# Optimization experiments

Measured on AMD Instinct MI355X. Metric: run time of the kernel, lower is better.

Reference implementation:

```python
import jax, jax.numpy as jnp
import numpy as np

N_HEAD = 8
HID = 256
V_DIM = HID // N_HEAD
IN_CH = 3
OUT_CH = 1
N_BLOCKS = 4
BATCH = 4
N_FULL = 4096
N_LAT = 1024
LOCALITIES = (3.0, 5.0, 5.0, 5.0, 5.0, 3.0)


def _linear(x, w, b):
    # eqx.nn.Linear convention: w is [out, in]
    return x @ w.T + b


def _pos_att(m_dist, x, r, weight, locality):
    # m_dist: [h, Nq, Nk]; x: [b, Nk, HID]; r: [h,1,1]; weight: [h, HID, V_DIM]
    scale = jnp.tan(0.25 * jnp.pi * (1 - 1e-07) * (1 + jnp.sin(r)))  # [h,1,1]
    sd = m_dist * scale  # [h, Nq, Nk]
    if locality <= 100:
        thr = jnp.percentile(sd, locality, axis=-1, keepdims=True)
        sd = jnp.where(sd <= thr, sd, jnp.inf)
    att = jax.nn.softmax(-sd, axis=-1)  # [h, Nq, Nk]
    value = jnp.einsum('bnj,hjk->bhnk', x, weight)  # [b, h, Nk, V_DIM]
    out = jnp.einsum('hjn,bhnk->bhjk', att, value)  # [b, h, Nq, V_DIM]
    out = out.transpose(0, 2, 1, 3).reshape(out.shape[0], out.shape[2], -1)  # [b, Nq, HID]
    return jax.nn.gelu(out)


def setup_inputs():
    key = jax.random.key(0)
    ks = jax.random.split(key, 16)
    def nrm(k, shape, scale=1.0):
        return jax.random.normal(k, shape, dtype=jnp.float32) * scale
    inv = float(1.0 / np.sqrt(HID))
    return {
        'x': nrm(ks[0], (BATCH, N_FULL, IN_CH)),
        'm_dist_down': jax.random.uniform(ks[1], (N_HEAD, N_LAT, N_FULL), dtype=jnp.float32),
        'm_dist_blocks': jax.random.uniform(ks[2], (N_BLOCKS, N_HEAD, N_LAT, N_LAT), dtype=jnp.float32),
        'm_dist_up': jax.random.uniform(ks[3], (N_HEAD, N_FULL, N_LAT), dtype=jnp.float32),
        'en_w': nrm(ks[4], (HID, IN_CH), float(1.0 / np.sqrt(IN_CH))),
        'en_b': jnp.zeros((HID,), jnp.float32),
        'down_r': nrm(ks[5], (N_HEAD, 1, 1)),
        'down_w': nrm(ks[6], (N_HEAD, HID, V_DIM), inv),
        'pa_r': nrm(ks[7], (N_BLOCKS, N_HEAD, 1, 1)),
        'pa_w': nrm(ks[8], (N_BLOCKS, N_HEAD, HID, V_DIM), inv),
        'mlp1_w': nrm(ks[9], (N_BLOCKS, HID, HID), inv),
        'mlp1_b': jnp.zeros((N_BLOCKS, HID), jnp.float32),
        'mlp2_w': nrm(ks[10], (N_BLOCKS, HID, HID), inv),
        'mlp2_b': jnp.zeros((N_BLOCKS, HID), jnp.float32),
        'res_w': nrm(ks[11], (N_BLOCKS, HID, HID), inv),
        'res_b': jnp.zeros((N_BLOCKS, HID), jnp.float32),
        'up_r': nrm(ks[12], (N_HEAD, 1, 1)),
        'up_w': nrm(ks[13], (N_HEAD, HID, V_DIM), inv),
        'de1_w': nrm(ks[14], (HID, HID), inv),
        'de1_b': jnp.zeros((HID,), jnp.float32),
        'de2_w': nrm(ks[15], (OUT_CH, HID), inv),
        'de2_b': jnp.zeros((OUT_CH,), jnp.float32),
    }


def reference(x, m_dist_down, m_dist_blocks, m_dist_up, en_w, en_b, down_r, down_w,
              pa_r, pa_w, mlp1_w, mlp1_b, mlp2_w, mlp2_b, res_w, res_b,
              up_r, up_w, de1_w, de1_b, de2_w, de2_b):
    # Encoder: lift + downsampling position-attention
    h = jax.nn.gelu(_linear(x, en_w, en_b))  # [b, N_FULL, HID]
    h = _pos_att(m_dist_down, h, down_r, down_w, LOCALITIES[0])  # [b, N_LAT, HID]
    # Processor blocks: PA -> MLP, plus linear residual, gelu
    for i in range(N_BLOCKS):
        pa = _pos_att(m_dist_blocks[i], h, pa_r[i], pa_w[i], LOCALITIES[1 + i])
        mlp = _linear(jax.nn.gelu(_linear(pa, mlp1_w[i], mlp1_b[i])), mlp2_w[i], mlp2_b[i])
        h = jax.nn.gelu(mlp + _linear(h, res_w[i], res_b[i]))
    # Decoder: upsampling position-attention + projection
    h = _pos_att(m_dist_up, h, up_r, up_w, LOCALITIES[-1])  # [b, N_FULL, HID]
    h = jax.nn.gelu(_linear(h, de1_w, de1_b))
    return _linear(h, de2_w, de2_b)  # [b, N_FULL, OUT_CH]
```

## Files before the change

kernel.cpp:

```cpp
#include <hip/hip_runtime.h>
#include <math.h>


typedef short bf16x8 __attribute__((ext_vector_type(8)));
typedef float f32x4 __attribute__((ext_vector_type(4)));

__device__ __forceinline__ float gelu_f(float x) {
  float x3 = x * x * x;
  float inner = x + 0.044715f * x3;
  float t = tanhf(0.7978845608028654f * inner);
  return x * (0.5f * (1.0f + t));
}

__device__ __forceinline__ unsigned short f2bf(float x) {
  union { float f; unsigned u; } v; v.f = x;
  return (unsigned short)((v.u + 0x7fffu + ((v.u >> 16) & 1u)) >> 16);
}
__device__ __forceinline__ float bf2f(unsigned short b) {
  union { unsigned u; float f; } v; v.u = ((unsigned)b) << 16; return v.f;
}
__device__ __forceinline__ void store_bf(unsigned short* hi, unsigned short* lo,
                                         size_t i, float v) {
  unsigned short h = f2bf(v);
  hi[i] = h;
  lo[i] = f2bf(v - bf2f(h));
}

struct PrepArgs {
  const float *mlp1, *mlp2, *res, *de1, *down, *pa, *up;
  unsigned short *rm_hi, *rm_lo, *val_hi, *val_lo;
};
__global__ __launch_bounds__(256) void k_prep(PrepArgs p) {
  int i = blockIdx.x * 256 + threadIdx.x;
  if (i < 851968) {
    const float* src; int off;
    if (i < 262144)      { src = p.mlp1; off = i; }
    else if (i < 524288) { src = p.mlp2; off = i - 262144; }
    else if (i < 786432) { src = p.res;  off = i - 524288; }
    else                 { src = p.de1;  off = i - 786432; }
    float x = src[off];
    store_bf(p.rm_hi, p.rm_lo, i, x);
  } else if (i < 1245184) {
    int ii = i - 851968;
    const float* src; int off;
    if (ii < 65536)       { src = p.down; off = ii; }
    else if (ii < 327680) { src = p.pa;   off = ii - 65536; }
    else                  { src = p.up;   off = ii - 327680; }
    int m = off >> 16, rem = off & 65535;
    int o = rem >> 8, j = rem & 255;
    float x = src[(size_t)m * 65536 + (o >> 5) * 8192 + j * 32 + (o & 31)];
    store_bf(p.val_hi, p.val_lo, ii, x);
  }
}

__global__ __launch_bounds__(256) void k_lift(const float* __restrict__ x,
                                              const float* __restrict__ w,
                                              const float* __restrict__ b,
                                              unsigned short* __restrict__ ohi,
                                              unsigned short* __restrict__ olo) {
  int gid = blockIdx.x * 256 + threadIdx.x;
  int m = gid >> 8, o = gid & 255;
  float a0 = x[m * 3 + 0], a1 = x[m * 3 + 1], a2 = x[m * 3 + 2];
  float acc = a0 * w[o * 3 + 0] + a1 * w[o * 3 + 1] + a2 * w[o * 3 + 2] + b[o];
  store_bf(ohi, olo, gid, gelu_f(acc));
}

template <int ACT, int ADDRES, int OBF16>
__global__ __launch_bounds__(256) void k_gemm(
    const unsigned short* __restrict__ Ahi, const unsigned short* __restrict__ Alo,
    const unsigned short* __restrict__ Whi, const unsigned short* __restrict__ Wlo,
    const float* __restrict__ bias, const float* __restrict__ D,
    float* __restrict__ C, unsigned short* __restrict__ Chi,
    unsigned short* __restrict__ Clo) {
  int t = threadIdx.x;
  int w = t >> 6, l = t & 63;
  int m0 = blockIdx.x * 64 + (w >> 1) * 32;
  int o0 = blockIdx.y * 64 + (w & 1) * 32;
  int fr = l & 15, fq = l >> 4;
  f32x4 acc[2][2] = {};
  size_t a0 = (size_t)(m0 + fr) * 256 + fq * 8;
  size_t a1 = a0 + 16 * 256;
  size_t b0 = (size_t)(o0 + fr) * 256 + fq * 8;
  size_t b1 = b0 + 16 * 256;
  for (int ks = 0; ks < 8; ++ks) {
    int k0 = ks * 32;
    bf16x8 A0h = *(const bf16x8*)(Ahi + a0 + k0);
    bf16x8 A0l = *(const bf16x8*)(Alo + a0 + k0);
    bf16x8 A1h = *(const bf16x8*)(Ahi + a1 + k0);
    bf16x8 A1l = *(const bf16x8*)(Alo + a1 + k0);
    bf16x8 B0h = *(const bf16x8*)(Whi + b0 + k0);
    bf16x8 B0l = *(const bf16x8*)(Wlo + b0 + k0);
    bf16x8 B1h = *(const bf16x8*)(Whi + b1 + k0);
    bf16x8 B1l = *(const bf16x8*)(Wlo + b1 + k0);
#define MFMA4(ACC, AH, AL, BH, BL)                                            \
  ACC = __builtin_amdgcn_mfma_f32_16x16x32_bf16(AH, BH, ACC, 0, 0, 0);        \
  ACC = __builtin_amdgcn_mfma_f32_16x16x32_bf16(AH, BL, ACC, 0, 0, 0);        \
  ACC = __builtin_amdgcn_mfma_f32_16x16x32_bf16(AL, BH, ACC, 0, 0, 0);        \
  ACC = __builtin_amdgcn_mfma_f32_16x16x32_bf16(AL, BL, ACC, 0, 0, 0);
    MFMA4(acc[0][0], A0h, A0l, B0h, B0l)
    MFMA4(acc[0][1], A0h, A0l, B1h, B1l)
    MFMA4(acc[1][0], A1h, A1l, B0h, B0l)
    MFMA4(acc[1][1], A1h, A1l, B1h, B1l)
#undef MFMA4
  }
  float bb[2];
  bb[0] = bias ? bias[o0 + fr] : 0.0f;
  bb[1] = bias ? bias[o0 + 16 + fr] : 0.0f;
#pragma unroll
  for (int i = 0; i < 2; ++i) {
#pragma unroll
    for (int jx = 0; jx < 2; ++jx) {
      int col = o0 + jx * 16 + fr;
#pragma unroll
      for (int r = 0; r < 4; ++r) {
        int rowi = m0 + i * 16 + fq * 4 + r;
        size_t oidx = (size_t)rowi * 256 + col;
        float v = acc[i][jx][r] + bb[jx];
        if (ADDRES) v += D[oidx];
        if (ACT) v = gelu_f(v);
        if (OBF16) store_bf(Chi, Clo, oidx, v);
        else C[oidx] = v;
      }
    }
  }
}

__global__ void k_scales(const float* __restrict__ down_r,
                         const float* __restrict__ pa_r,
                         const float* __restrict__ up_r,
                         float* __restrict__ scales) {
  int t = threadIdx.x;
  if (t >= 48) return;
  float rv;
  if (t < 8) rv = down_r[t];
  else if (t < 40) rv = pa_r[t - 8];
  else rv = up_r[t - 40];
  double rd = (double)rv;
  float s1 = (float)sin(rd);
  float u = 1.0f + s1;
  float vc = (float)(0.7853981633974483 * (1.0 - 1e-7));
  float wf = vc * u;
  scales[t] = (float)tan((double)wf);
}

template <int N, int CAP>
__global__ __launch_bounds__(256) void k_wselpv(
    const float* __restrict__ mdist, const float* __restrict__ scales,
    int sc_off, int Nq, int k_lo, float hw, float lw, float frac,
    const float* __restrict__ V, int Nk,
    unsigned short* __restrict__ out_hi, unsigned short* __restrict__ out_lo) {
  constexpr int CH = N / 256;
  constexpr int SMAX = (CAP + 63) / 64;
  __shared__ float cv[4][CAP];
  __shared__ int ci[4][CAP];
  __shared__ int ccnt[4];
  __shared__ float svsel[4][2];
  __shared__ float swin[4][32];

  int tid = threadIdx.x;
  int w = tid >> 6, l = tid & 63;
  int row = blockIdx.x * 4 + w;
  int h = row / Nq, j = row - h * Nq;
  float scale = scales[sc_off + h];
  const float4* mrow4 = (const float4*)(mdist + (size_t)row * N);

  float lmin = INFINITY, lmax = -INFINITY;
#pragma unroll
  for (int e = 0; e < CH; ++e) {
    float4 v = mrow4[l + 64 * e];
    lmin = fminf(lmin, fminf(fminf(v.x, v.y), fminf(v.z, v.w)));
    lmax = fmaxf(lmax, fmaxf(fmaxf(v.x, v.y), fmaxf(v.z, v.w)));
  }
#pragma unroll
  for (int off = 32; off > 0; off >>= 1) {
    lmin = fminf(lmin, __shfl_xor(lmin, off));
    lmax = fmaxf(lmax, __shfl_xor(lmax, off));
  }
  float rmin = lmin, rmax = lmax;

  int K = 0;
  float inv_total = 1.0f;
  if (rmax > rmin) {
    float range = rmax - rmin;
    float margin = fmaxf(fabsf(rmax) * 1e-6f, 1e-30f);
    float rtop = rmax + margin;
    float wtop = rmin + range * frac;
    if (!(wtop > rmin)) wtop = rtop;
    float v_lo = rmin, v_hi = rmin;
    int count = 0;
    float xv[SMAX];
    for (int it = 0; it < 20; ++it) {
      if (l == 0) ccnt[w] = 0;
#pragma unroll
      for (int e = 0; e < CH; ++e) {
        float4 v = mrow4[l + 64 * e];
        int i0 = 4 * (l + 64 * e);
        if (v.x < wtop) { int p = atomicAdd(&ccnt[w], 1); if (p < CAP) { cv[w][p] = v.x; ci[w][p] = i0; } }
        if (v.y < wtop) { int p = atomicAdd(&ccnt[w], 1); if (p < CAP) { cv[w][p] = v.y; ci[w][p] = i0 + 1; } }
        if (v.z < wtop) { int p = atomicAdd(&ccnt[w], 1); if (p < CAP) { cv[w][p] = v.z; ci[w][p] = i0 + 2; } }
        if (v.w < wtop) { int p = atomicAdd(&ccnt[w], 1); if (p < CAP) { cv[w][p] = v.w; ci[w][p] = i0 + 3; } }
      }
      count = ccnt[w];
      if (count < k_lo + 2) { wtop = fminf(rmin + (wtop - rmin) * 3.0f, rtop); continue; }
      if (count > CAP)      { wtop = rmin + (wtop - rmin) * 0.6f; continue; }

#pragma unroll
      for (int s = 0; s < SMAX; ++s) {
        int slot = l + 64 * s;
        xv[s] = (slot < count) ? cv[w][slot] : INFINITY;
      }
      float wlo = rmin, whi = wtop;
      int rbase = 0, cntw = count;
      int found = 0, degen = 0;
      for (int bs = 0; bs < 32; ++bs) {
        if (cntw <= 24) break;
        float mid = 0.5f * (wlo + whi);
        if (!(mid > wlo && mid < whi)) { degen = 1; break; }
        int c4 = 0;
#pragma unroll
        for (int s = 0; s < SMAX; ++s) c4 += (xv[s] >= wlo && xv[s] < mid) ? 1 : 0;
#pragma unroll
        for (int off = 32; off > 0; off >>= 1) c4 += __shfl_xor(c4, off);
        int rrel = k_lo - rbase;
        if (rrel + 1 < c4) { whi = mid; cntw = c4; }
        else if (rrel >= c4) { wlo = mid; rbase += c4; cntw -= c4; }
        else {
          float mx = -INFINITY, mn = INFINITY;
#pragma unroll
          for (int s = 0; s < SMAX; ++s) {
            float v = xv[s];
            if (v >= wlo && v < mid) mx = fmaxf(mx, v);
            if (v >= mid && v < whi) mn = fminf(mn, v);
          }
#pragma unroll
          for (int off = 32; off > 0; off >>= 1) {
            mx = fmaxf(mx, __shfl_xor(mx, off));
            mn = fminf(mn, __shfl_xor(mn, off));
          }
          v_lo = mx; v_hi = mn; found = 1;
          break;
        }
      }
      if (!found) {
        if (!degen && cntw <= 32) {
          if (l == 0) ccnt[w] = 0;
#pragma unroll
          for (int s = 0; s < SMAX; ++s) {
            float v = xv[s];
            if (v >= wlo && v < whi) {
              int p = atomicAdd(&ccnt[w], 1);
              if (p < 32) swin[w][p] = v;
            }
          }
          int m = ccnt[w];
          if (m > 32) m = 32;
          float myv = (l < m) ? swin[w][l] : INFINITY;
          int clt = 0, ceq = 0;
          for (int jj = 0; jj < m; ++jj) {
            float y = swin[w][jj];
            clt += (y < myv) ? 1 : 0;
            ceq += (y == myv) ? 1 : 0;
          }
          int rr = k_lo - rbase;
          if (l < m) {
            if (clt <= rr && rr < clt + ceq) svsel[w][0] = myv;
            if (clt <= rr + 1 && rr + 1 < clt + ceq) svsel[w][1] = myv;
          }
          v_lo = svsel[w][0];
          v_hi = svsel[w][1];
        } else {
          int clt[SMAX], ceq[SMAX];
#pragma unroll
          for (int s = 0; s < SMAX; ++s) { clt[s] = 0; ceq[s] = 0; }
          for (int jj = 0; jj < count; ++jj) {
            float y = cv[w][jj];
#pragma unroll
            for (int s = 0; s < SMAX; ++s) {
              clt[s] += (y < xv[s]) ? 1 : 0;
              ceq[s] += (y == xv[s]) ? 1 : 0;
            }
          }
#pragma unroll
          for (int s = 0; s < SMAX; ++s) {
            int slot = l + 64 * s;
            if (slot < count) {
              if (clt[s] <= k_lo && k_lo < clt[s] + ceq[s]) svsel[w][0] = xv[s];
              if (clt[s] <= k_lo + 1 && k_lo + 1 < clt[s] + ceq[s]) svsel[w][1] = xv[s];
            }
          }
          v_lo = svsel[w][0];
          v_hi = svsel[w][1];
        }
      }
      float vlos0 = __fmul_rn(v_lo, scale);
      float vhis0 = __fmul_rn(v_hi, scale);
      float thr0 = __fadd_rn(__fmul_rn(vlos0, lw), __fmul_rn(vhis0, hw));
      if (__fmul_rn(wtop, scale) <= thr0) {
        wtop = fminf(rmin + (wtop - rmin) * 3.0f, rtop);
        continue;
      }
      break;
    }

    float vlos = __fmul_rn(v_lo, scale);
    float vhis = __fmul_rn(v_hi, scale);
    float thr = __fadd_rn(__fmul_rn(vlos, lw), __fmul_rn(vhis, hw));
    float rmins = __fmul_rn(rmin, scale);

    int oi[SMAX]; int kp[SMAX];
#pragma unroll
    for (int s = 0; s < SMAX; ++s) {
      int slot = l + 64 * s;
      oi[s] = 0; kp[s] = 0;
      if (slot < count) {
        oi[s] = ci[w][slot];
        kp[s] = (__fmul_rn(xv[s], scale) <= thr) ? 1 : 0;
      }
    }
    int base = 0;
    float lsum = 0.0f;
    unsigned long long mlt = (l == 0) ? 0ull : (~0ull >> (64 - l));
#pragma unroll
    for (int s = 0; s < SMAX; ++s) {
      unsigned long long bal = __ballot(kp[s] != 0);
      int pos = base + (int)__popcll(bal & mlt);
      if (kp[s]) {
        float e0 = expf(__fsub_rn(rmins, __fmul_rn(xv[s], scale)));
        cv[w][pos] = e0;
        ci[w][pos] = oi[s];
        lsum += e0;
      }
      base += (int)__popcll(bal);
    }
    K = base;
#pragma unroll
    for (int off = 32; off > 0; off >>= 1) lsum += __shfl_xor(lsum, off);
    inv_total = 1.0f / lsum;
  } else {
    K = 0;
    inv_total = 1.0f / (float)Nk;
  }

  int bh = l >> 5, c = l & 31;
  int hcol = h * 32 + c;
  const float* Vb0 = V + (size_t)bh * Nk * 256;
  const float* Vb1 = V + (size_t)(bh + 2) * Nk * 256;
  float acc0 = 0.0f, acc1 = 0.0f;
  if (K > 0) {
    for (int e = 0; e < K; ++e) {
      float we = cv[w][e];
      int n = ci[w][e];
      size_t o = (size_t)n * 256 + hcol;
      acc0 = fmaf(we, Vb0[o], acc0);
      acc1 = fmaf(we, Vb1[o], acc1);
    }
  } else {
    for (int n = 0; n < Nk; ++n) {
      size_t o = (size_t)n * 256 + hcol;
      acc0 += Vb0[o];
      acc1 += Vb1[o];
    }
  }
  size_t o0i = ((size_t)bh * Nq + j) * 256 + hcol;
  size_t o1i = ((size_t)(bh + 2) * Nq + j) * 256 + hcol;
  store_bf(out_hi, out_lo, o0i, gelu_f(acc0 * inv_total));
  store_bf(out_hi, out_lo, o1i, gelu_f(acc1 * inv_total));
}

__global__ __launch_bounds__(256) void k_de2(const float* __restrict__ A,
                                             const float* __restrict__ w,
                                             const float* __restrict__ b,
                                             float* __restrict__ out) {
  int t = threadIdx.x;
  int row = blockIdx.x * 4 + (t >> 6);
  int lane = t & 63;
  const float* ar = A + (size_t)row * 256;
  float s = 0.0f;
  for (int i = lane; i < 256; i += 64) s = fmaf(ar[i], w[i], s);
#pragma unroll
  for (int off = 32; off > 0; off >>= 1) s += __shfl_down(s, off);
  if (lane == 0) out[row] = s + b[0];
}

struct SelParams { int k_lo; float hw, lw, frac; };
static SelParams sel_params(double q, int N) {
  SelParams p;
  float idx_q = (float)(q / 100.0);
  float pos = idx_q * (float)(N - 1);
  float lo = floorf(pos);
  p.k_lo = (int)lo;
  p.hw = pos - lo;
  p.lw = 1.0f - p.hw;
  float need = (float)(p.k_lo + 2);
  p.frac = (need + 6.0f * sqrtf(need) + 8.0f) / (float)N;
  return p;
}

extern "C" void kernel_launch(void* const* d_in, const int* in_sizes, int n_in,
                              void* d_out, int out_size, void* d_ws, size_t ws_size,
                              hipStream_t stream) {
  const float* x      = (const float*)d_in[0];
  const float* mdd    = (const float*)d_in[1];
  const float* mdb    = (const float*)d_in[2];
  const float* mdu    = (const float*)d_in[3];
  const float* en_w   = (const float*)d_in[4];
  const float* en_b   = (const float*)d_in[5];
  const float* down_r = (const float*)d_in[6];
  const float* down_w = (const float*)d_in[7];
  const float* pa_r   = (const float*)d_in[8];
  const float* pa_w   = (const float*)d_in[9];
  const float* mlp1_w = (const float*)d_in[10];
  const float* mlp1_b = (const float*)d_in[11];
  const float* mlp2_w = (const float*)d_in[12];
  const float* mlp2_b = (const float*)d_in[13];
  const float* res_w  = (const float*)d_in[14];
  const float* res_b  = (const float*)d_in[15];
  const float* up_r   = (const float*)d_in[16];
  const float* up_w   = (const float*)d_in[17];
  const float* de1_w  = (const float*)d_in[18];
  const float* de1_b  = (const float*)d_in[19];
  const float* de2_w  = (const float*)d_in[20];
  const float* de2_b  = (const float*)d_in[21];
  float* out = (float*)d_out;
  char* base = (char*)d_ws;

  float* val               = (float*)base;
  float* t2                = (float*)(base + 16777216);
  unsigned short* hfull_hi = (unsigned short*)(base + 20971520);
  unsigned short* hfull_lo = (unsigned short*)(base + 29360128);
  unsigned short* paout_hi = (unsigned short*)(base + 37748736);
  unsigned short* paout_lo = (unsigned short*)(base + 46137344);
  unsigned short* hlat_hi  = (unsigned short*)(base + 54525952);
  unsigned short* hlat_lo  = (unsigned short*)(base + 56623104);
  unsigned short* t1_hi    = (unsigned short*)(base + 58720256);
  unsigned short* t1_lo    = (unsigned short*)(base + 60817408);
  unsigned short* wrm_hi   = (unsigned short*)(base + 62914560);
  unsigned short* wrm_lo   = (unsigned short*)(base + 64618496);
  unsigned short* wval_hi  = (unsigned short*)(base + 66322432);
  unsigned short* wval_lo  = (unsigned short*)(base + 67108864);
  float* scales            = (float*)(base + 67895296);

  k_scales<<<1, 64, 0, stream>>>(down_r, pa_r, up_r, scales);

  PrepArgs pa;
  pa.mlp1 = mlp1_w; pa.mlp2 = mlp2_w; pa.res = res_w; pa.de1 = de1_w;
  pa.down = down_w; pa.pa = pa_w; pa.up = up_w;
  pa.rm_hi = wrm_hi; pa.rm_lo = wrm_lo; pa.val_hi = wval_hi; pa.val_lo = wval_lo;
  k_prep<<<4864, 256, 0, stream>>>(pa);

  k_lift<<<16384, 256, 0, stream>>>(x, en_w, en_b, hfull_hi, hfull_lo);

  SelParams pd = sel_params(3.0, 4096);
  k_gemm<0, 0, 0><<<dim3(256, 4), 256, 0, stream>>>(
      hfull_hi, hfull_lo, wval_hi, wval_lo, nullptr, nullptr, val, nullptr, nullptr);
  k_wselpv<4096, 256><<<2048, 256, 0, stream>>>(
      mdd, scales, 0, 1024, pd.k_lo, pd.hw, pd.lw, pd.frac, val, 4096, hlat_hi, hlat_lo);

  SelParams pb = sel_params(5.0, 1024);
  for (int i = 0; i < 4; i++) {
    k_gemm<0, 0, 0><<<dim3(64, 4), 256, 0, stream>>>(
        hlat_hi, hlat_lo, wval_hi + 65536 + i * 65536, wval_lo + 65536 + i * 65536,
        nullptr, nullptr, val, nullptr, nullptr);
    k_wselpv<1024, 256><<<2048, 256, 0, stream>>>(
        mdb + (size_t)i * 8388608, scales, 8 + i * 8, 1024, pb.k_lo, pb.hw, pb.lw,
        pb.frac, val, 1024, paout_hi, paout_lo);
    k_gemm<1, 0, 1><<<dim3(64, 4), 256, 0, stream>>>(
        paout_hi, paout_lo, wrm_hi + i * 65536, wrm_lo + i * 65536,
        mlp1_b + i * 256, nullptr, nullptr, t1_hi, t1_lo);
    k_gemm<0, 0, 0><<<dim3(64, 4), 256, 0, stream>>>(
        hlat_hi, hlat_lo, wrm_hi + 524288 + i * 65536, wrm_lo + 524288 + i * 65536,
        res_b + i * 256, nullptr, t2, nullptr, nullptr);
    k_gemm<1, 1, 1><<<dim3(64, 4), 256, 0, stream>>>(
        t1_hi, t1_lo, wrm_hi + 262144 + i * 65536, wrm_lo + 262144 + i * 65536,
        mlp2_b + i * 256, t2, nullptr, hlat_hi, hlat_lo);
  }

  SelParams pu = sel_params(3.0, 1024);
  k_gemm<0, 0, 0><<<dim3(64, 4), 256, 0, stream>>>(
      hlat_hi, hlat_lo, wval_hi + 327680, wval_lo + 327680, nullptr, nullptr,
      val, nullptr, nullptr);
  k_wselpv<1024, 192><<<8192, 256, 0, stream>>>(
      mdu, scales, 40, 4096, pu.k_lo, pu.hw, pu.lw, pu.frac, val, 1024,
      paout_hi, paout_lo);

  k_gemm<1, 0, 0><<<dim3(256, 4), 256, 0, stream>>>(
      paout_hi, paout_lo, wrm_hi + 786432, wrm_lo + 786432, de1_b, nullptr,
      val, nullptr, nullptr);
  k_de2<<<4096, 256, 0, stream>>>(val, de2_w, de2_b, out);
}
```

Measured before the change: 548.7 us.

## Fuse candidate filtering into min/max pass and pack selection value/index pairs

The selection kernel now estimates the threshold from a sampled first chunk and collects candidates during the min/max pass, so the usual case skips a second full read of the distance row. Value and index are packed into a single float2 shared array, the candidate capacity for the downsampling rows is raised, and the weighted-value gather reads two adjacent columns per lane for one batch instead of strided columns across two batches. The scale computation is folded into the weight-prep kernel, removing one launch. In exchange, shared memory per block grows, and a poor sampled estimate forces extra refilter passes.

```diff
diff --git a/kernel.cpp b/kernel.cpp
--- a/kernel.cpp
+++ b/kernel.cpp
@@ -28,9 +28,26 @@
 
 struct PrepArgs {
   const float *mlp1, *mlp2, *res, *de1, *down, *pa, *up;
+  const float *down_r, *pa_r, *up_r;
   unsigned short *rm_hi, *rm_lo, *val_hi, *val_lo;
+  float* scales;
 };
 __global__ __launch_bounds__(256) void k_prep(PrepArgs p) {
+  if (blockIdx.x == 4864) {
+    int t = threadIdx.x;
+    if (t >= 48) return;
+    float rv;
+    if (t < 8) rv = p.down_r[t];
+    else if (t < 40) rv = p.pa_r[t - 8];
+    else rv = p.up_r[t - 40];
+    double rd = (double)rv;
+    float s1 = (float)sin(rd);
+    float u = 1.0f + s1;
+    float vc = (float)(0.7853981633974483 * (1.0 - 1e-7));
+    float wf = vc * u;
+    p.scales[t] = (float)tan((double)wf);
+    return;
+  }
   int i = blockIdx.x * 256 + threadIdx.x;
   if (i < 851968) {
     const float* src; int off;
@@ -125,34 +142,15 @@
   }
 }
 
-__global__ void k_scales(const float* __restrict__ down_r,
-                         const float* __restrict__ pa_r,
-                         const float* __restrict__ up_r,
-                         float* __restrict__ scales) {
-  int t = threadIdx.x;
-  if (t >= 48) return;
-  float rv;
-  if (t < 8) rv = down_r[t];
-  else if (t < 40) rv = pa_r[t - 8];
-  else rv = up_r[t - 40];
-  double rd = (double)rv;
-  float s1 = (float)sin(rd);
-  float u = 1.0f + s1;
-  float vc = (float)(0.7853981633974483 * (1.0 - 1e-7));
-  float wf = vc * u;
-  scales[t] = (float)tan((double)wf);
-}
-
 template <int N, int CAP>
 __global__ __launch_bounds__(256) void k_wselpv(
     const float* __restrict__ mdist, const float* __restrict__ scales,
-    int sc_off, int Nq, int k_lo, float hw, float lw, float frac,
+    int sc_off, int Nq, int k_lo, float hw, float lw, float fracx,
     const float* __restrict__ V, int Nk,
     unsigned short* __restrict__ out_hi, unsigned short* __restrict__ out_lo) {
   constexpr int CH = N / 256;
-  constexpr int SMAX = (CAP + 63) / 64;
-  __shared__ float cv[4][CAP];
-  __shared__ int ci[4][CAP];
+  constexpr int SMAX = CAP / 64;
+  __shared__ float2 cd[4][CAP];
   __shared__ int ccnt[4];
   __shared__ float svsel[4][2];
   __shared__ float swin[4][32];
@@ -164,12 +162,28 @@
   float scale = scales[sc_off + h];
   const float4* mrow4 = (const float4*)(mdist + (size_t)row * N);
 
+  float4 s0 = mrow4[l];
+  float smin = fminf(fminf(s0.x, s0.y), fminf(s0.z, s0.w));
+  float smax = fmaxf(fmaxf(s0.x, s0.y), fmaxf(s0.z, s0.w));
+#pragma unroll
+  for (int off = 32; off > 0; off >>= 1) {
+    smin = fminf(smin, __shfl_xor(smin, off));
+    smax = fmaxf(smax, __shfl_xor(smax, off));
+  }
+  float est = smin + (smax - smin) * fracx;
+
+  if (l == 0) ccnt[w] = 0;
   float lmin = INFINITY, lmax = -INFINITY;
 #pragma unroll
   for (int e = 0; e < CH; ++e) {
     float4 v = mrow4[l + 64 * e];
     lmin = fminf(lmin, fminf(fminf(v.x, v.y), fminf(v.z, v.w)));
     lmax = fmaxf(lmax, fmaxf(fmaxf(v.x, v.y), fmaxf(v.z, v.w)));
+    int i0 = 4 * (l + 64 * e);
+    if (v.x < est) { int p = atomicAdd(&ccnt[w], 1); if (p < CAP) cd[w][p] = make_float2(v.x, __int_as_float(i0)); }
+    if (v.y < est) { int p = atomicAdd(&ccnt[w], 1); if (p < CAP) cd[w][p] = make_float2(v.y, __int_as_float(i0 + 1)); }
+    if (v.z < est) { int p = atomicAdd(&ccnt[w], 1); if (p < CAP) cd[w][p] = make_float2(v.z, __int_as_float(i0 + 2)); }
+    if (v.w < est) { int p = atomicAdd(&ccnt[w], 1); if (p < CAP) cd[w][p] = make_float2(v.w, __int_as_float(i0 + 3)); }
   }
 #pragma unroll
   for (int off = 32; off > 0; off >>= 1) {
@@ -181,33 +195,46 @@
   int K = 0;
   float inv_total = 1.0f;
   if (rmax > rmin) {
-    float range = rmax - rmin;
     float margin = fmaxf(fabsf(rmax) * 1e-6f, 1e-30f);
     float rtop = rmax + margin;
-    float wtop = rmin + range * frac;
+    float wtop = est;
     if (!(wtop > rmin)) wtop = rtop;
     float v_lo = rmin, v_hi = rmin;
     int count = 0;
-    float xv[SMAX];
+    float xv[SMAX]; int oi[SMAX];
+    bool refilter = (wtop != est);
     for (int it = 0; it < 20; ++it) {
-      if (l == 0) ccnt[w] = 0;
-#pragma unroll
-      for (int e = 0; e < CH; ++e) {
-        float4 v = mrow4[l + 64 * e];
-        int i0 = 4 * (l + 64 * e);
-        if (v.x < wtop) { int p = atomicAdd(&ccnt[w], 1); if (p < CAP) { cv[w][p] = v.x; ci[w][p] = i0; } }
-        if (v.y < wtop) { int p = atomicAdd(&ccnt[w], 1); if (p < CAP) { cv[w][p] = v.y; ci[w][p] = i0 + 1; } }
-        if (v.z < wtop) { int p = atomicAdd(&ccnt[w], 1); if (p < CAP) { cv[w][p] = v.z; ci[w][p] = i0 + 2; } }
-        if (v.w < wtop) { int p = atomicAdd(&ccnt[w], 1); if (p < CAP) { cv[w][p] = v.w; ci[w][p] = i0 + 3; } }
+      if (refilter) {
+        if (l == 0) ccnt[w] = 0;
+#pragma unroll
+        for (int e = 0; e < CH; ++e) {
+          float4 v = mrow4[l + 64 * e];
+          int i0 = 4 * (l + 64 * e);
+          if (v.x < wtop) { int p = atomicAdd(&ccnt[w], 1); if (p < CAP) cd[w][p] = make_float2(v.x, __int_as_float(i0)); }
+          if (v.y < wtop) { int p = atomicAdd(&ccnt[w], 1); if (p < CAP) cd[w][p] = make_float2(v.y, __int_as_float(i0 + 1)); }
+          if (v.z < wtop) { int p = atomicAdd(&ccnt[w], 1); if (p < CAP) cd[w][p] = make_float2(v.z, __int_as_float(i0 + 2)); }
+          if (v.w < wtop) { int p = atomicAdd(&ccnt[w], 1); if (p < CAP) cd[w][p] = make_float2(v.w, __int_as_float(i0 + 3)); }
+        }
+        refilter = false;
       }
       count = ccnt[w];
-      if (count < k_lo + 2) { wtop = fminf(rmin + (wtop - rmin) * 3.0f, rtop); continue; }
-      if (count > CAP)      { wtop = rmin + (wtop - rmin) * 0.6f; continue; }
+      if (count < k_lo + 2) {
+        wtop = fminf(rmin + fmaxf((wtop - rmin) * 3.0f, (rtop - rmin) * 0.001f), rtop);
+        refilter = true;
+        continue;
+      }
+      if (count > CAP) {
+        wtop = rmin + (wtop - rmin) * 0.6f;
+        refilter = true;
+        continue;
+      }
 
 #pragma unroll
       for (int s = 0; s < SMAX; ++s) {
         int slot = l + 64 * s;
-        xv[s] = (slot < count) ? cv[w][slot] : INFINITY;
+        float2 c2 = cd[w][slot];
+        xv[s] = (slot < count) ? c2.x : INFINITY;
+        oi[s] = __float_as_int(c2.y);
       }
       float wlo = rmin, whi = wtop;
       int rbase = 0, cntw = count;
@@ -268,12 +295,13 @@
           }
           v_lo = svsel[w][0];
           v_hi = svsel[w][1];
+          if (l == 0) ccnt[w] = count;
         } else {
           int clt[SMAX], ceq[SMAX];
 #pragma unroll
           for (int s = 0; s < SMAX; ++s) { clt[s] = 0; ceq[s] = 0; }
           for (int jj = 0; jj < count; ++jj) {
-            float y = cv[w][jj];
+            float y = cd[w][jj].x;
 #pragma unroll
             for (int s = 0; s < SMAX; ++s) {
               clt[s] += (y < xv[s]) ? 1 : 0;
@@ -296,7 +324,8 @@
       float vhis0 = __fmul_rn(v_hi, scale);
       float thr0 = __fadd_rn(__fmul_rn(vlos0, lw), __fmul_rn(vhis0, hw));
       if (__fmul_rn(wtop, scale) <= thr0) {
-        wtop = fminf(rmin + (wtop - rmin) * 3.0f, rtop);
+        wtop = fminf(rmin + fmaxf((wtop - rmin) * 3.0f, (rtop - rmin) * 0.001f), rtop);
+        refilter = true;
         continue;
       }
       break;
@@ -307,15 +336,11 @@
     float thr = __fadd_rn(__fmul_rn(vlos, lw), __fmul_rn(vhis, hw));
     float rmins = __fmul_rn(rmin, scale);
 
-    int oi[SMAX]; int kp[SMAX];
+    int kp[SMAX];
 #pragma unroll
     for (int s = 0; s < SMAX; ++s) {
       int slot = l + 64 * s;
-      oi[s] = 0; kp[s] = 0;
-      if (slot < count) {
-        oi[s] = ci[w][slot];
-        kp[s] = (__fmul_rn(xv[s], scale) <= thr) ? 1 : 0;
-      }
+      kp[s] = (slot < count) ? ((__fmul_rn(xv[s], scale) <= thr) ? 1 : 0) : 0;
     }
     int base = 0;
     float lsum = 0.0f;
@@ -326,8 +351,7 @@
       int pos = base + (int)__popcll(bal & mlt);
       if (kp[s]) {
         float e0 = expf(__fsub_rn(rmins, __fmul_rn(xv[s], scale)));
-        cv[w][pos] = e0;
-        ci[w][pos] = oi[s];
+        cd[w][pos] = make_float2(e0, __int_as_float(oi[s]));
         lsum += e0;
       }
       base += (int)__popcll(bal);
@@ -341,30 +365,28 @@
     inv_total = 1.0f / (float)Nk;
   }
 
-  int bh = l >> 5, c = l & 31;
-  int hcol = h * 32 + c;
-  const float* Vb0 = V + (size_t)bh * Nk * 256;
-  const float* Vb1 = V + (size_t)(bh + 2) * Nk * 256;
+  int b = l >> 4, c4 = (l & 15) * 2;
+  int hcol = h * 32 + c4;
+  const float* Vb = V + (size_t)b * Nk * 256;
   float acc0 = 0.0f, acc1 = 0.0f;
   if (K > 0) {
     for (int e = 0; e < K; ++e) {
-      float we = cv[w][e];
-      int n = ci[w][e];
-      size_t o = (size_t)n * 256 + hcol;
-      acc0 = fmaf(we, Vb0[o], acc0);
-      acc1 = fmaf(we, Vb1[o], acc1);
+      float2 wi = cd[w][e];
+      int n = __float_as_int(wi.y);
+      const float2 vv = *(const float2*)(Vb + (size_t)n * 256 + hcol);
+      acc0 = fmaf(wi.x, vv.x, acc0);
+      acc1 = fmaf(wi.x, vv.y, acc1);
     }
   } else {
     for (int n = 0; n < Nk; ++n) {
-      size_t o = (size_t)n * 256 + hcol;
-      acc0 += Vb0[o];
-      acc1 += Vb1[o];
+      const float2 vv = *(const float2*)(Vb + (size_t)n * 256 + hcol);
+      acc0 += vv.x;
+      acc1 += vv.y;
     }
   }
-  size_t o0i = ((size_t)bh * Nq + j) * 256 + hcol;
-  size_t o1i = ((size_t)(bh + 2) * Nq + j) * 256 + hcol;
-  store_bf(out_hi, out_lo, o0i, gelu_f(acc0 * inv_total));
-  store_bf(out_hi, out_lo, o1i, gelu_f(acc1 * inv_total));
+  size_t oidx = ((size_t)b * Nq + j) * 256 + hcol;
+  store_bf(out_hi, out_lo, oidx, gelu_f(acc0 * inv_total));
+  store_bf(out_hi, out_lo, oidx + 1, gelu_f(acc1 * inv_total));
 }
 
 __global__ __launch_bounds__(256) void k_de2(const float* __restrict__ A,
@@ -382,7 +404,7 @@
   if (lane == 0) out[row] = s + b[0];
 }
 
-struct SelParams { int k_lo; float hw, lw, frac; };
+struct SelParams { int k_lo; float hw, lw, fracx; };
 static SelParams sel_params(double q, int N) {
   SelParams p;
   float idx_q = (float)(q / 100.0);
@@ -392,7 +414,8 @@
   p.hw = pos - lo;
   p.lw = 1.0f - p.hw;
   float need = (float)(p.k_lo + 2);
-  p.frac = (need + 6.0f * sqrtf(need) + 8.0f) / (float)N;
+  float frac = (need + 6.0f * sqrtf(need) + 8.0f) / (float)N;
+  p.fracx = 1.6f * frac;
   return p;
 }
 
@@ -440,21 +463,21 @@
   unsigned short* wval_lo  = (unsigned short*)(base + 67108864);
   float* scales            = (float*)(base + 67895296);
 
-  k_scales<<<1, 64, 0, stream>>>(down_r, pa_r, up_r, scales);
-
   PrepArgs pa;
   pa.mlp1 = mlp1_w; pa.mlp2 = mlp2_w; pa.res = res_w; pa.de1 = de1_w;
   pa.down = down_w; pa.pa = pa_w; pa.up = up_w;
+  pa.down_r = down_r; pa.pa_r = pa_r; pa.up_r = up_r;
   pa.rm_hi = wrm_hi; pa.rm_lo = wrm_lo; pa.val_hi = wval_hi; pa.val_lo = wval_lo;
-  k_prep<<<4864, 256, 0, stream>>>(pa);
+  pa.scales = scales;
+  k_prep<<<4865, 256, 0, stream>>>(pa);
 
   k_lift<<<16384, 256, 0, stream>>>(x, en_w, en_b, hfull_hi, hfull_lo);
 
   SelParams pd = sel_params(3.0, 4096);
   k_gemm<0, 0, 0><<<dim3(256, 4), 256, 0, stream>>>(
       hfull_hi, hfull_lo, wval_hi, wval_lo, nullptr, nullptr, val, nullptr, nullptr);
-  k_wselpv<4096, 256><<<2048, 256, 0, stream>>>(
-      mdd, scales, 0, 1024, pd.k_lo, pd.hw, pd.lw, pd.frac, val, 4096, hlat_hi, hlat_lo);
+  k_wselpv<4096, 512><<<2048, 256, 0, stream>>>(
+      mdd, scales, 0, 1024, pd.k_lo, pd.hw, pd.lw, pd.fracx, val, 4096, hlat_hi, hlat_lo);
 
   SelParams pb = sel_params(5.0, 1024);
   for (int i = 0; i < 4; i++) {
@@ -463,7 +486,7 @@
         nullptr, nullptr, val, nullptr, nullptr);
     k_wselpv<1024, 256><<<2048, 256, 0, stream>>>(
         mdb + (size_t)i * 8388608, scales, 8 + i * 8, 1024, pb.k_lo, pb.hw, pb.lw,
-        pb.frac, val, 1024, paout_hi, paout_lo);
+        pb.fracx, val, 1024, paout_hi, paout_lo);
     k_gemm<1, 0, 1><<<dim3(64, 4), 256, 0, stream>>>(
         paout_hi, paout_lo, wrm_hi + i * 65536, wrm_lo + i * 65536,
         mlp1_b + i * 256, nullptr, nullptr, t1_hi, t1_lo);
@@ -480,7 +503,7 @@
       hlat_hi, hlat_lo, wval_hi + 327680, wval_lo + 327680, nullptr, nullptr,
       val, nullptr, nullptr);
   k_wselpv<1024, 192><<<8192, 256, 0, stream>>>(
-      mdu, scales, 40, 4096, pu.k_lo, pu.hw, pu.lw, pu.frac, val, 1024,
+      mdu, scales, 40, 4096, pu.k_lo, pu.hw, pu.lw, pu.fracx, val, 1024,
       paout_hi, paout_lo);
 
   k_gemm<1, 0, 0><<<dim3(256, 4), 256, 0, stream>>>(
```

New measurement: 612.3 us. +11.6%, slower.
